# Performance work log

Hardware: AMD Instinct MI355X
Metric: run time of the kernel (lower is better)

## Reference

```python
import jax, jax.numpy as jnp
import numpy as np

T, B, L = 4, 8192, 50
VOCAB, D = 100000, 128


def setup_inputs() -> dict:
    key = jax.random.key(0)
    ks = jax.random.split(key, 10)
    inp = {
        "indices": jax.random.randint(ks[0], (T, B, L), 0, VOCAB, dtype=jnp.int32),
        "lengths": jax.random.randint(ks[1], (T, B), 0, L, dtype=jnp.int32),
        "tables": jax.random.normal(ks[2], (T, VOCAB, D), dtype=jnp.float32) * 0.02,
        "W1": jax.random.normal(ks[3], (D, D), dtype=jnp.float32) * (1.0 / np.sqrt(D)),
        "b1": jax.random.normal(ks[4], (D,), dtype=jnp.float32) * 0.01,
        "W2": jax.random.normal(ks[5], (D, D), dtype=jnp.float32) * (1.0 / np.sqrt(D)),
        "b2": jax.random.normal(ks[6], (D,), dtype=jnp.float32) * 0.01,
        "W3": jax.random.normal(ks[7], (D, D), dtype=jnp.float32) * (1.0 / np.sqrt(D)),
        "b3": jax.random.normal(ks[8], (D,), dtype=jnp.float32) * 0.01,
    }
    return inp


def reference(indices, lengths, tables, W1, b1, W2, b2, W3, b3):
    # Per-table jagged gather + SUM pooling (EmbeddingBagCollection default).
    t, b, l = indices.shape
    emb = jax.vmap(lambda tab, idx: tab[idx])(tables, indices)  # [T,B,L,D]
    mask = (jnp.arange(l, dtype=lengths.dtype) < lengths[..., None])[..., None]
    pooled = jnp.sum(jnp.where(mask, emb, jnp.zeros((), emb.dtype)), axis=2)  # [T,B,D]
    # torch.cat over dict values concatenates along dim 0 -> [T*B, D]
    x = pooled.reshape(t * b, -1)
    # nn.Sequential of three Linear(D, D) layers, no activation
    x = x @ W1.T + b1
    x = x @ W2.T + b2
    x = x @ W3.T + b3
    return x
```

## Files before the change

### kernel.cpp

```cpp
#include <hip/hip_runtime.h>


#define T_ 4
#define B_ 8192
#define L_ 50
#define VOCAB_ 100000
#define D_ 128
#define ROWS 16
#define PSTRIDE 20

#define WS_A1 0
#define WS_C1 16384
#define WS_M  16512
#define WS_C  32896

__global__ __launch_bounds__(128) void combine1(const float* __restrict__ W1,
                                                const float* __restrict__ W2,
                                                const float* __restrict__ b1,
                                                const float* __restrict__ b2,
                                                float* __restrict__ ws) {
  const int j = threadIdx.x;
  const int i = blockIdx.x;
  if (i < D_) {
    float acc = 0.f;
    for (int k = 0; k < D_; ++k)
      acc += W1[k * D_ + i] * W2[j * D_ + k];
    ws[WS_A1 + i * D_ + j] = acc;
  } else {
    float acc = b2[j];
    for (int k = 0; k < D_; ++k)
      acc += b1[k] * W2[j * D_ + k];
    ws[WS_C1 + j] = acc;
  }
}

__global__ __launch_bounds__(128) void combine2(const float* __restrict__ W3,
                                                const float* __restrict__ b3,
                                                const float* __restrict__ ws_in,
                                                float* __restrict__ ws) {
  const int j = threadIdx.x;
  const int i = blockIdx.x;
  if (i < D_) {
    float acc = 0.f;
    for (int k = 0; k < D_; ++k)
      acc += ws_in[WS_A1 + i * D_ + k] * W3[j * D_ + k];
    ws[WS_M + i * D_ + j] = acc;
  } else {
    float acc = b3[j];
    for (int k = 0; k < D_; ++k)
      acc += ws_in[WS_C1 + k] * W3[j * D_ + k];
    ws[WS_C + j] = acc;
  }
}

__global__ __launch_bounds__(256) void fused(const int* __restrict__ indices,
                                             const int* __restrict__ lengths,
                                             const float* __restrict__ tables,
                                             const float* __restrict__ ws,
                                             float* __restrict__ out) {
  __shared__ __align__(16) float pooledT[D_][PSTRIDE];
  __shared__ int   idx_sh[ROWS][L_];
  __shared__ float c_sh[D_];
  __shared__ int   len_sh[ROWS];

  const int tid = threadIdx.x;
  const int g0  = blockIdx.x * ROWS;

  for (int k = tid; k < ROWS * L_; k += 256)
    idx_sh[k / L_][k % L_] = indices[g0 * L_ + k];
  if (tid < D_)   c_sh[tid]  = ws[WS_C + tid];
  if (tid < ROWS) len_sh[tid] = lengths[g0 + tid];
  __syncthreads();

  {
    const int lane = tid & 63;
    const int wv   = tid >> 6;
    const int d0   = lane * 2;
    const int t    = g0 >> 13;
    const float* __restrict__ tab = tables + (size_t)t * (VOCAB_ * D_) + d0;

    for (int q = 0; q < ROWS / 4; ++q) {
      const int r   = wv * 4 + q;
      const int len = len_sh[r];
      const int* __restrict__ il = idx_sh[r];
      float ax = 0.f, ay = 0.f;
      int l = 0;
      for (; l + 7 < len; l += 8) {
        const int i0 = il[l + 0], i1 = il[l + 1], i2 = il[l + 2], i3 = il[l + 3];
        const int i4 = il[l + 4], i5 = il[l + 5], i6 = il[l + 6], i7 = il[l + 7];
        const float2 v0 = *(const float2*)(tab + (size_t)i0 * D_);
        const float2 v1 = *(const float2*)(tab + (size_t)i1 * D_);
        const float2 v2 = *(const float2*)(tab + (size_t)i2 * D_);
        const float2 v3 = *(const float2*)(tab + (size_t)i3 * D_);
        const float2 v4 = *(const float2*)(tab + (size_t)i4 * D_);
        const float2 v5 = *(const float2*)(tab + (size_t)i5 * D_);
        const float2 v6 = *(const float2*)(tab + (size_t)i6 * D_);
        const float2 v7 = *(const float2*)(tab + (size_t)i7 * D_);
        ax += v0.x; ay += v0.y;  ax += v1.x; ay += v1.y;
        ax += v2.x; ay += v2.y;  ax += v3.x; ay += v3.y;
        ax += v4.x; ay += v4.y;  ax += v5.x; ay += v5.y;
        ax += v6.x; ay += v6.y;  ax += v7.x; ay += v7.y;
      }
      for (; l + 1 < len; l += 2) {
        const float2 va = *(const float2*)(tab + (size_t)il[l] * D_);
        const float2 vb = *(const float2*)(tab + (size_t)il[l + 1] * D_);
        ax += va.x; ay += va.y;  ax += vb.x; ay += vb.y;
      }
      if (l < len) {
        const float2 v = *(const float2*)(tab + (size_t)il[l] * D_);
        ax += v.x; ay += v.y;
      }
      pooledT[d0][r]     = ax;
      pooledT[d0 + 1][r] = ay;
    }
  }
  __syncthreads();

  const int j = tid & (D_ - 1);
  const int rbase = (tid >> 7) * 8;
  const float* Mg = ws + WS_M;
  float acc[8];
#pragma unroll
  for (int r = 0; r < 8; ++r) acc[r] = c_sh[j];
#pragma unroll 4
  for (int i = 0; i < D_; ++i) {
    const float m = Mg[i * D_ + j];
    const float4 p0 = *(const float4*)&pooledT[i][rbase];
    const float4 p1 = *(const float4*)&pooledT[i][rbase + 4];
    acc[0] += p0.x * m; acc[1] += p0.y * m; acc[2] += p0.z * m; acc[3] += p0.w * m;
    acc[4] += p1.x * m; acc[5] += p1.y * m; acc[6] += p1.z * m; acc[7] += p1.w * m;
  }
#pragma unroll
  for (int r = 0; r < 8; ++r)
    out[(size_t)(g0 + rbase + r) * D_ + j] = acc[r];
}

extern "C" void kernel_launch(void* const* d_in, const int* in_sizes, int n_in,
                              void* d_out, int out_size, void* d_ws, size_t ws_size,
                              hipStream_t stream) {
  const int*   indices = (const int*)d_in[0];
  const int*   lengths = (const int*)d_in[1];
  const float* tables  = (const float*)d_in[2];
  const float* W1      = (const float*)d_in[3];
  const float* b1      = (const float*)d_in[4];
  const float* W2      = (const float*)d_in[5];
  const float* b2      = (const float*)d_in[6];
  const float* W3      = (const float*)d_in[7];
  const float* b3      = (const float*)d_in[8];
  float*       out     = (float*)d_out;
  float*       ws      = (float*)d_ws;

  combine1<<<D_ + 1, D_, 0, stream>>>(W1, W2, b1, b2, ws);
  combine2<<<D_ + 1, D_, 0, stream>>>(W3, b3, ws, ws);
  fused<<<(T_ * B_) / ROWS, 256, 0, stream>>>(indices, lengths, tables, ws, out);
}
```

Measured before the change: 342.4 us.

## Merge weight-combine kernels and balance bag gathers with per-block atomic work queue

Folds the two weight-precombination kernels into one, computing W1·W2 rows in shared memory before multiplying by W3, which removes a launch and a workspace round trip. The fused gather kernel halves rows per block. Each wavefront now takes bags dynamically through a shared-memory atomic counter, so waves that draw short bags pick up more work instead of idling. The pooled buffer moves to row-major layout with float2 stores, and the matmul does 4 rows per thread. The tradeoff is extra atomic and shuffle overhead per bag and less reuse of M loads per block.

```diff
diff --git a/kernel.cpp b/kernel.cpp
--- a/kernel.cpp
+++ b/kernel.cpp
@@ -6,50 +6,42 @@
 #define L_ 50
 #define VOCAB_ 100000
 #define D_ 128
-#define ROWS 16
-#define PSTRIDE 20
+#define ROWS 8
+#define NBAGS (T_ * B_)
 
-#define WS_A1 0
-#define WS_C1 16384
-#define WS_M  16512
-#define WS_C  32896
+#define WS_M  0
+#define WS_C  16384
 
-__global__ __launch_bounds__(128) void combine1(const float* __restrict__ W1,
-                                                const float* __restrict__ W2,
-                                                const float* __restrict__ b1,
-                                                const float* __restrict__ b2,
-                                                float* __restrict__ ws) {
+__global__ __launch_bounds__(128) void combine(const float* __restrict__ W1,
+                                               const float* __restrict__ W2,
+                                               const float* __restrict__ W3,
+                                               const float* __restrict__ b1,
+                                               const float* __restrict__ b2,
+                                               const float* __restrict__ b3,
+                                               float* __restrict__ ws) {
+  __shared__ float a1[D_];
   const int j = threadIdx.x;
   const int i = blockIdx.x;
   if (i < D_) {
     float acc = 0.f;
     for (int k = 0; k < D_; ++k)
       acc += W1[k * D_ + i] * W2[j * D_ + k];
-    ws[WS_A1 + i * D_ + j] = acc;
+    a1[j] = acc;
+    __syncthreads();
+    float m = 0.f;
+    for (int k = 0; k < D_; ++k)
+      m += a1[k] * W3[j * D_ + k];
+    ws[WS_M + i * D_ + j] = m;
   } else {
-    float acc = b2[j];
+    float c1 = b2[j];
     for (int k = 0; k < D_; ++k)
-      acc += b1[k] * W2[j * D_ + k];
-    ws[WS_C1 + j] = acc;
-  }
-}
-
-__global__ __launch_bounds__(128) void combine2(const float* __restrict__ W3,
-                                                const float* __restrict__ b3,
-                                                const float* __restrict__ ws_in,
-                                                float* __restrict__ ws) {
-  const int j = threadIdx.x;
-  const int i = blockIdx.x;
-  if (i < D_) {
-    float acc = 0.f;
+      c1 += b1[k] * W2[j * D_ + k];
+    a1[j] = c1;
+    __syncthreads();
+    float c = b3[j];
     for (int k = 0; k < D_; ++k)
-      acc += ws_in[WS_A1 + i * D_ + k] * W3[j * D_ + k];
-    ws[WS_M + i * D_ + j] = acc;
-  } else {
-    float acc = b3[j];
-    for (int k = 0; k < D_; ++k)
-      acc += ws_in[WS_C1 + k] * W3[j * D_ + k];
-    ws[WS_C + j] = acc;
+      c += a1[k] * W3[j * D_ + k];
+    ws[WS_C + j] = c;
   }
 }
 
@@ -58,31 +50,33 @@
                                              const float* __restrict__ tables,
                                              const float* __restrict__ ws,
                                              float* __restrict__ out) {
-  __shared__ __align__(16) float pooledT[D_][PSTRIDE];
-  __shared__ int   idx_sh[ROWS][L_];
-  __shared__ float c_sh[D_];
-  __shared__ int   len_sh[ROWS];
+  __shared__ __align__(16) float pooled_sh[ROWS][D_];
+  __shared__ int idx_sh[ROWS][L_];
+  __shared__ int len_sh[ROWS];
+  __shared__ int bag_ctr;
 
   const int tid = threadIdx.x;
   const int g0  = blockIdx.x * ROWS;
 
+  if (tid == 0) bag_ctr = 0;
   for (int k = tid; k < ROWS * L_; k += 256)
     idx_sh[k / L_][k % L_] = indices[g0 * L_ + k];
-  if (tid < D_)   c_sh[tid]  = ws[WS_C + tid];
   if (tid < ROWS) len_sh[tid] = lengths[g0 + tid];
   __syncthreads();
 
   {
     const int lane = tid & 63;
-    const int wv   = tid >> 6;
     const int d0   = lane * 2;
     const int t    = g0 >> 13;
     const float* __restrict__ tab = tables + (size_t)t * (VOCAB_ * D_) + d0;
 
-    for (int q = 0; q < ROWS / 4; ++q) {
-      const int r   = wv * 4 + q;
-      const int len = len_sh[r];
-      const int* __restrict__ il = idx_sh[r];
+    for (;;) {
+      int pos = 0;
+      if (lane == 0) pos = atomicAdd(&bag_ctr, 1);
+      pos = __shfl(pos, 0, 64);
+      if (pos >= ROWS) break;
+      const int len = len_sh[pos];
+      const int* __restrict__ il = idx_sh[pos];
       float ax = 0.f, ay = 0.f;
       int l = 0;
       for (; l + 7 < len; l += 8) {
@@ -110,29 +104,28 @@
         const float2 v = *(const float2*)(tab + (size_t)il[l] * D_);
         ax += v.x; ay += v.y;
       }
-      pooledT[d0][r]     = ax;
-      pooledT[d0 + 1][r] = ay;
+      *(float2*)&pooled_sh[pos][d0] = make_float2(ax, ay);
     }
   }
   __syncthreads();
 
-  const int j = tid & (D_ - 1);
-  const int rbase = (tid >> 7) * 8;
-  const float* Mg = ws + WS_M;
-  float acc[8];
-#pragma unroll
-  for (int r = 0; r < 8; ++r) acc[r] = c_sh[j];
+  const int j  = tid & (D_ - 1);
+  const int rh = (tid >> 7) * 4;
+  const float* __restrict__ Mg = ws + WS_M;
+  const float cj = ws[WS_C + j];
+  float acc0 = cj, acc1 = cj, acc2 = cj, acc3 = cj;
 #pragma unroll 4
   for (int i = 0; i < D_; ++i) {
     const float m = Mg[i * D_ + j];
-    const float4 p0 = *(const float4*)&pooledT[i][rbase];
-    const float4 p1 = *(const float4*)&pooledT[i][rbase + 4];
-    acc[0] += p0.x * m; acc[1] += p0.y * m; acc[2] += p0.z * m; acc[3] += p0.w * m;
-    acc[4] += p1.x * m; acc[5] += p1.y * m; acc[6] += p1.z * m; acc[7] += p1.w * m;
+    acc0 += pooled_sh[rh + 0][i] * m;
+    acc1 += pooled_sh[rh + 1][i] * m;
+    acc2 += pooled_sh[rh + 2][i] * m;
+    acc3 += pooled_sh[rh + 3][i] * m;
   }
-#pragma unroll
-  for (int r = 0; r < 8; ++r)
-    out[(size_t)(g0 + rbase + r) * D_ + j] = acc[r];
+  out[(size_t)(g0 + rh + 0) * D_ + j] = acc0;
+  out[(size_t)(g0 + rh + 1) * D_ + j] = acc1;
+  out[(size_t)(g0 + rh + 2) * D_ + j] = acc2;
+  out[(size_t)(g0 + rh + 3) * D_ + j] = acc3;
 }
 
 extern "C" void kernel_launch(void* const* d_in, const int* in_sizes, int n_in,
@@ -150,7 +143,6 @@
   float*       out     = (float*)d_out;
   float*       ws      = (float*)d_ws;
 
-  combine1<<<D_ + 1, D_, 0, stream>>>(W1, W2, b1, b2, ws);
-  combine2<<<D_ + 1, D_, 0, stream>>>(W3, b3, ws, ws);
-  fused<<<(T_ * B_) / ROWS, 256, 0, stream>>>(indices, lengths, tables, ws, out);
+  combine<<<D_ + 1, D_, 0, stream>>>(W1, W2, W3, b1, b2, b3, ws);
+  fused<<<NBAGS / ROWS, 256, 0, stream>>>(indices, lengths, tables, ws, out);
 }
```

Result: no change. 341.0 us (-0.4%).
